# Performance work log

Hardware: AMD Instinct MI355X
Metric: run time of the kernel (lower is better)

The kernel has to match this reference:

```python
import jax, jax.numpy as jnp
import numpy as np

WET_MIX = 0.3
FEEDBACK = 0.4
ROOM_SIZE = 0.5
NUM_REFL = 8
NUM_HEADS = 4

# Delay kernel table: int(delay) in {0,1,2,>=3} -> kernel_size {identity,3,5,7}.
# A k-tap kernel with padding k//2 == the same kernel zero-padded to 7 taps with padding 3.
def _gauss7(ks):
    g = np.exp(-np.linspace(-2.0, 2.0, ks) ** 2)
    g = g / g.sum()
    out = np.zeros(7, np.float32)
    s = (7 - ks) // 2
    out[s:s + ks] = g
    return out
_delta = np.zeros(7, np.float32); _delta[3] = 1.0
K_TABLE = jnp.asarray(np.stack([_delta, _gauss7(3), _gauss7(5), _gauss7(7)]))  # [4,7]


def _conv2d(x, w, b, pad):
    y = jax.lax.conv_general_dilated(x, w, (1, 1), [(pad, pad), (pad, pad)],
                                     dimension_numbers=('NCHW', 'OIHW', 'NCHW'))
    return y + b[None, :, None, None]


def _delay_line(x, kern7):
    # vertical depthwise Gaussian blur, same for every (batch, channel) plane
    b, c, h, w = x.shape
    k = kern7.reshape(1, 1, 7, 1)
    y = jax.lax.conv_general_dilated(x.reshape(b * c, 1, h, w), k, (1, 1), [(3, 3), (0, 0)],
                                     dimension_numbers=('NCHW', 'OIHW', 'NCHW'))
    return y.reshape(b, c, h, w)


def _forward(x, refl_w, refl_d, sc_w, sc_b, fb_w, fb_b, d1_w, d1_b, d2_w, d2_b,
             in_proj_w, in_proj_b, out_proj_w, out_proj_b, oc_w, oc_b):
    B, C, H, W = x.shape
    scaled = refl_d * ROOM_SIZE
    kidx = jnp.clip(jnp.floor(scaled).astype(jnp.int32), 0, 3)  # int(delay) detaches grad, as in torch

    wet = jnp.zeros_like(x)
    fb_buf = x * 0.1
    spatial = _conv2d(x, sc_w, sc_b, 1)  # [B,2C,H,W]

    for i in range(NUM_REFL):
        refl = _delay_line(fb_buf, K_TABLE[kidx[i]])
        refl = _conv2d(refl, fb_w, fb_b, 1)
        damp = jax.nn.sigmoid(_conv2d(jax.nn.silu(_conv2d(refl, d1_w, d1_b, 0)), d2_w, d2_b, 0))
        refl = refl * damp
        weight = jax.nn.sigmoid(refl_w[i]) * (0.8 ** i)
        wet = wet + refl * weight
        fb_buf = fb_buf + refl * (FEEDBACK * 0.1)

    # MultiheadAttention over L = H*W tokens, embed_dim=C=4, 4 heads (head_dim=1)
    L = H * W
    hd = C // NUM_HEADS
    wet_flat = wet.reshape(B, C, L).transpose(0, 2, 1)           # [B,L,C]
    qkv = wet_flat @ in_proj_w.T + in_proj_b                     # [B,L,3C]
    q, k, v = jnp.split(qkv, 3, axis=-1)
    def heads(t):
        return t.reshape(B, L, NUM_HEADS, hd).transpose(0, 2, 1, 3)  # [B,H,L,hd]
    q, k, v = heads(q), heads(k), heads(v)
    scores = jnp.einsum('bhqd,bhkd->bhqk', q, k) / np.sqrt(hd).astype(np.float32)
    attn = jax.nn.softmax(scores, axis=-1)
    o = jnp.einsum('bhqk,bhkd->bhqd', attn, v)
    o = o.transpose(0, 2, 1, 3).reshape(B, L, C) @ out_proj_w.T + out_proj_b
    wet2 = o.transpose(0, 2, 1).reshape(B, C, H, W)

    combined = jnp.concatenate([spatial, wet2], axis=1)          # [B,3C,H,W]
    processed_wet = _conv2d(combined, oc_w, oc_b, 0)
    return x * (1.0 - WET_MIX) + processed_wet * WET_MIX


def setup_inputs() -> dict:
    key = jax.random.key(0)
    ks = jax.random.split(key, 16)
    B, C, H, W = 2, 4, 64, 64
    f32 = jnp.float32
    return {
        'x': jax.random.normal(ks[0], (B, C, H, W), f32),
        'refl_w': jax.random.normal(ks[1], (8,), f32) * 0.1,
        'refl_d': jax.random.randint(ks[2], (8,), 1, 16).astype(f32),
        'sc_w': jax.random.normal(ks[3], (2 * C, C, 3, 3), f32) * 0.1,
        'sc_b': jnp.zeros((2 * C,), f32),
        'fb_w': jax.random.normal(ks[4], (C, C, 3, 3), f32) * 0.1,
        'fb_b': jnp.zeros((C,), f32),
        'd1_w': jax.random.normal(ks[5], (C // 2, C, 1, 1), f32) * 0.3,
        'd1_b': jnp.zeros((C // 2,), f32),
        'd2_w': jax.random.normal(ks[6], (C, C // 2, 1, 1), f32) * 0.3,
        'd2_b': jnp.zeros((C,), f32),
        'in_proj_w': jax.random.normal(ks[7], (3 * C, C), f32) * 0.3,
        'in_proj_b': jnp.zeros((3 * C,), f32),
        'out_proj_w': jax.random.normal(ks[8], (C, C), f32) * 0.3,
        'out_proj_b': jnp.zeros((C,), f32),
        'oc_w': jax.random.normal(ks[9], (C, 3 * C, 1, 1), f32) * 0.2,
        'oc_b': jnp.zeros((C,), f32),
    }


def reference(x, refl_w, refl_d, sc_w, sc_b, fb_w, fb_b, d1_w, d1_b, d2_w, d2_b,
              in_proj_w, in_proj_b, out_proj_w, out_proj_b, oc_w, oc_b):
    return _forward(x, refl_w, refl_d, sc_w, sc_b, fb_w, fb_b, d1_w, d1_b, d2_w, d2_b,
                    in_proj_w, in_proj_b, out_proj_w, out_proj_b, oc_w, oc_b)
```

## Files before the change

kernel.cpp:

```cpp
#include <hip/hip_runtime.h>
#include <math.h>


#define ZERO4 make_float4(0.f, 0.f, 0.f, 0.f)

__device__ __forceinline__ float sigf(float v) { return 1.0f / (1.0f + __expf(-v)); }

__device__ __forceinline__ float dppL(float v) {
    return __int_as_float(__builtin_amdgcn_mov_dpp(__float_as_int(v), 0x138, 0xf, 0xf, true));
}
__device__ __forceinline__ float dppR(float v) {
    return __int_as_float(__builtin_amdgcn_mov_dpp(__float_as_int(v), 0x130, 0xf, 0xf, true));
}
__device__ __forceinline__ float4 shL4(float4 v) {
    return make_float4(dppL(v.x), dppL(v.y), dppL(v.z), dppL(v.w));
}
__device__ __forceinline__ float4 shR4(float4 v) {
    return make_float4(dppR(v.x), dppR(v.y), dppR(v.z), dppR(v.w));
}

__device__ __forceinline__ void tap(float4& a, const float4 t, const float* wp) {
    a.x += wp[0]   * t.x + wp[9]    * t.y + wp[18]    * t.z + wp[27]    * t.w;
    a.y += wp[36]  * t.x + wp[36+9] * t.y + wp[36+18] * t.z + wp[36+27] * t.w;
    a.z += wp[72]  * t.x + wp[72+9] * t.y + wp[72+18] * t.z + wp[72+27] * t.w;
    a.w += wp[108] * t.x + wp[108+9]* t.y + wp[108+18]* t.z + wp[108+27]* t.w;
}

__global__ __launch_bounds__(1024, 1) void reverb_qkv_kernel(
    const float* __restrict__ x,
    const float* __restrict__ refl_w,
    const float* __restrict__ refl_d,
    const float* __restrict__ fb_w,
    const float* __restrict__ fb_b,
    const float* __restrict__ d1_w,
    const float* __restrict__ d1_b,
    const float* __restrict__ d2_w,
    const float* __restrict__ d2_b,
    const float* __restrict__ ipw,
    const float* __restrict__ ipb,
    float* __restrict__ Qg, float* __restrict__ Kg, float* __restrict__ Vg)
{
    __shared__ float4 P [18 * 64];
    __shared__ float4 BL[18 * 64];
    __shared__ float4 WT[2 * 64];
    __shared__ float  GT[3][8];

    const int blk   = blockIdx.x;
    const int batch = blk >> 5;
    const int own0  = (blk & 31) << 1;
    const int LB    = own0 - 8;
    const int tid   = threadIdx.x;
    const int wy    = tid >> 6;
    const int r     = tid & 63;

    if (tid < 3) {
        const int rr = tid + 1;
        const int ks = 2 * rr + 1;
        const int s  = (7 - ks) >> 1;
        const double step = 4.0 / (double)(ks - 1);
        double g[7]; double sum = 0.0;
        for (int t = 0; t < 7; ++t) {
            if (t < ks) { double u = -2.0 + step * (double)t; g[t] = exp(-u * u); sum += g[t]; }
        }
        for (int t = 0; t < 7; ++t) GT[tid][t] = 0.0f;
        for (int t = 0; t < ks; ++t) GT[tid][s + t] = (float)(g[t] / sum);
    }

    for (int idx = tid; idx < 18 * 64; idx += 1024) {
        const int lc  = idx >> 6;
        const int row = idx & 63;
        const int gc  = LB + lc;
        float4 v = ZERO4;
        if (gc >= 0 && gc < 64) {
            const int base = batch * 16384 + row * 64 + gc;
            v.x = 0.1f * x[base];
            v.y = 0.1f * x[base + 4096];
            v.z = 0.1f * x[base + 8192];
            v.w = 0.1f * x[base + 12288];
        }
        P[idx] = v;
    }
    __syncthreads();

    double w8 = 1.0;
    for (int j = 0; j < 8; ++j) {
        int kidx = (int)floorf(refl_d[j] * 0.5f);
        kidx = kidx < 0 ? 0 : (kidx > 3 ? 3 : kidx);
        float kv[7];
        #pragma unroll
        for (int u = 0; u < 7; ++u) {
            const float dv = (u == 3) ? 1.0f : 0.0f;
            kv[u] = (kidx == 0) ? dv : GT[kidx - 1][u];
        }
        const float wgt = sigf(refl_w[j]) * (float)w8;

        const int clo = max(0, own0 - (7 - j));
        const int chi = min(64, own0 + 2 + (7 - j));

        const int lcA   = (clo - 1) - LB;
        const int nBlur = (chi + 1) - (clo - 1);
        for (int t = wy; t < nBlur; t += 16) {
            const int lc = lcA + t;
            const int gc = LB + lc;
            float4 b = ZERO4;
            if (gc >= 0 && gc < 64) {
                const float4 v  = P[lc * 64 + r];
                const float4 l1 = shL4(v),  l2 = shL4(l1), l3 = shL4(l2);
                const float4 r1 = shR4(v),  r2 = shR4(r1), r3 = shR4(r2);
                b.x = kv[0]*l3.x + kv[1]*l2.x + kv[2]*l1.x + kv[3]*v.x
                    + kv[4]*r1.x + kv[5]*r2.x + kv[6]*r3.x;
                b.y = kv[0]*l3.y + kv[1]*l2.y + kv[2]*l1.y + kv[3]*v.y
                    + kv[4]*r1.y + kv[5]*r2.y + kv[6]*r3.y;
                b.z = kv[0]*l3.z + kv[1]*l2.z + kv[2]*l1.z + kv[3]*v.z
                    + kv[4]*r1.z + kv[5]*r2.z + kv[6]*r3.z;
                b.w = kv[0]*l3.w + kv[1]*l2.w + kv[2]*l1.w + kv[3]*v.w
                    + kv[4]*r1.w + kv[5]*r2.w + kv[6]*r3.w;
            }
            BL[lc * 64 + r] = b;
        }
        __syncthreads();

        const int c = clo + wy;
        if (wy < chi - clo) {
            const int lc = c - LB;
            const float4 bm = BL[(lc - 1) * 64 + r];
            const float4 bc = BL[lc * 64 + r];
            const float4 bp = BL[(lc + 1) * 64 + r];

            float4 acc = make_float4(fb_b[0], fb_b[1], fb_b[2], fb_b[3]);
            tap(acc, shL4(bm), fb_w + 0);  tap(acc, shL4(bc), fb_w + 1);  tap(acc, shL4(bp), fb_w + 2);
            tap(acc, bm,       fb_w + 3);  tap(acc, bc,       fb_w + 4);  tap(acc, bp,       fb_w + 5);
            tap(acc, shR4(bm), fb_w + 6);  tap(acc, shR4(bc), fb_w + 7);  tap(acc, shR4(bp), fb_w + 8);

            float4 rr = acc;
            float h0 = d1_b[0] + d1_w[0]*rr.x + d1_w[1]*rr.y + d1_w[2]*rr.z + d1_w[3]*rr.w;
            float h1 = d1_b[1] + d1_w[4]*rr.x + d1_w[5]*rr.y + d1_w[6]*rr.z + d1_w[7]*rr.w;
            h0 = h0 * sigf(h0);
            h1 = h1 * sigf(h1);
            const float d0  = sigf(d2_b[0] + d2_w[0]*h0 + d2_w[1]*h1);
            const float d1v = sigf(d2_b[1] + d2_w[2]*h0 + d2_w[3]*h1);
            const float d2v = sigf(d2_b[2] + d2_w[4]*h0 + d2_w[5]*h1);
            const float d3v = sigf(d2_b[3] + d2_w[6]*h0 + d2_w[7]*h1);
            rr.x *= d0; rr.y *= d1v; rr.z *= d2v; rr.w *= d3v;

            const float4 oldfb = P[lc * 64 + r];
            P[lc * 64 + r] = make_float4(oldfb.x + 0.04f*rr.x, oldfb.y + 0.04f*rr.y,
                                         oldfb.z + 0.04f*rr.z, oldfb.w + 0.04f*rr.w);

            if (c >= own0 && c < own0 + 2) {
                const int widx = (c - own0) * 64 + r;
                float4 wv = make_float4(wgt*rr.x, wgt*rr.y, wgt*rr.z, wgt*rr.w);
                if (j > 0) {
                    const float4 old = WT[widx];
                    wv.x += old.x; wv.y += old.y; wv.z += old.z; wv.w += old.w;
                }
                WT[widx] = wv;
            }
        }
        __syncthreads();
        w8 *= 0.8;
    }

    if (tid < 128) {
        const int row = tid & 63;
        const int oc  = tid >> 6;
        const int c   = own0 + oc;
        const float4 wv = WT[oc * 64 + row];
        #pragma unroll
        for (int h = 0; h < 4; ++h) {
            const float q = ipb[h]
                + ipw[h*4+0]*wv.x + ipw[h*4+1]*wv.y
                + ipw[h*4+2]*wv.z + ipw[h*4+3]*wv.w;
            const float k = ipb[4+h]
                + ipw[(4+h)*4+0]*wv.x + ipw[(4+h)*4+1]*wv.y
                + ipw[(4+h)*4+2]*wv.z + ipw[(4+h)*4+3]*wv.w;
            const float v = ipb[8+h]
                + ipw[(8+h)*4+0]*wv.x + ipw[(8+h)*4+1]*wv.y
                + ipw[(8+h)*4+2]*wv.z + ipw[(8+h)*4+3]*wv.w;
            const int o = (batch * 4 + h) * 4096 + row * 64 + c;
            Qg[o] = q; Kg[o] = k; Vg[o] = v;
        }
    }
}

__global__ __launch_bounds__(256) void attn_kernel(
    const float* __restrict__ Qg, const float* __restrict__ Kg,
    const float* __restrict__ Vg,
    float* __restrict__ PN, float* __restrict__ PD, float* __restrict__ PM)
{
    __shared__ float2 KV[1024];
    __shared__ float  wred[8];
    __shared__ float  partN[256], partD[256];

    const int bh  = blockIdx.x >> 8;
    const int sub = (blockIdx.x >> 2) & 63;
    const int ks  = blockIdx.x & 3;
    const int tid = threadIdx.x;

    const float* Kp = Kg + bh * 4096 + ks * 1024;
    const float* Vp = Vg + bh * 4096 + ks * 1024;

    float pmax = -3.0e38f, pmin = 3.0e38f;
    #pragma unroll
    for (int t = tid; t < 1024; t += 256) {
        const float kk = Kp[t];
        const float vv = Vp[t];
        KV[t] = make_float2(kk, vv);
        pmax = fmaxf(pmax, kk);
        pmin = fminf(pmin, kk);
    }
    #pragma unroll
    for (int off = 32; off > 0; off >>= 1) {
        pmax = fmaxf(pmax, __shfl_xor(pmax, off, 64));
        pmin = fminf(pmin, __shfl_xor(pmin, off, 64));
    }
    if ((tid & 63) == 0) { wred[tid >> 6] = pmax; wred[4 + (tid >> 6)] = pmin; }
    __syncthreads();
    const float kmax = fmaxf(fmaxf(wred[0], wred[1]), fmaxf(wred[2], wred[3]));
    const float kmin = fminf(fminf(wred[4], wred[5]), fminf(wred[6], wred[7]));

    const int ql = tid & 63;
    const int kh = __builtin_amdgcn_readfirstlane(tid >> 6);
    const int qi = sub * 64 + ql;

    const float L2E = 1.4426950408889634f;
    const float q  = Qg[bh * 4096 + qi];
    const float q2 = q * L2E;
    const float m2 = ((q >= 0.0f) ? q * kmax : q * kmin) * L2E;
    const float nm2 = -m2;

    const float4* KV4 = (const float4*)KV;
    const int base4 = kh * 128;

    float num0 = 0.f, num1 = 0.f, den0 = 0.f, den1 = 0.f;
    #pragma unroll 8
    for (int j = 0; j < 128; ++j) {
        const float4 f = KV4[base4 + j];
        const float e0 = __builtin_amdgcn_exp2f(__fmaf_rn(q2, f.x, nm2));
        den0 += e0;  num0 = __fmaf_rn(e0, f.y, num0);
        const float e1 = __builtin_amdgcn_exp2f(__fmaf_rn(q2, f.z, nm2));
        den1 += e1;  num1 = __fmaf_rn(e1, f.w, num1);
    }
    partN[tid] = num0 + num1;
    partD[tid] = den0 + den1;
    __syncthreads();
    if (tid < 64) {
        const float n = partN[tid] + partN[tid + 64] + partN[tid + 128] + partN[tid + 192];
        const float d = partD[tid] + partD[tid + 64] + partD[tid + 128] + partD[tid + 192];
        const int o = bh * 16384 + ks * 4096 + sub * 64 + tid;
        PN[o] = n;
        PD[o] = d;
        PM[o] = m2;
    }
}

__global__ __launch_bounds__(128) void final_kernel(
    const float* __restrict__ x,
    const float* __restrict__ sc_w, const float* __restrict__ sc_b,
    const float* __restrict__ opw,  const float* __restrict__ opb,
    const float* __restrict__ ocw,  const float* __restrict__ ocb,
    const float* __restrict__ PN,   const float* __restrict__ PD,
    const float* __restrict__ PM,   float* __restrict__ out)
{
    const int g   = blockIdx.x * 128 + threadIdx.x;
    const int b   = g >> 12;
    const int pix = g & 4095;
    const int y   = pix >> 6;
    const int xc  = pix & 63;

    float xin[4][3][3];
    #pragma unroll
    for (int ic = 0; ic < 4; ++ic)
        #pragma unroll
        for (int ky = 0; ky < 3; ++ky)
            #pragma unroll
            for (int kx = 0; kx < 3; ++kx) {
                const int yy = y + ky - 1, xx = xc + kx - 1;
                xin[ic][ky][kx] = (yy >= 0 && yy < 64 && xx >= 0 && xx < 64)
                                    ? x[(b * 4 + ic) * 4096 + yy * 64 + xx] : 0.f;
            }

    float sp[8];
    #pragma unroll
    for (int oc = 0; oc < 8; ++oc) {
        float a = sc_b[oc];
        #pragma unroll
        for (int ic = 0; ic < 4; ++ic)
            #pragma unroll
            for (int ky = 0; ky < 3; ++ky)
                #pragma unroll
                for (int kx = 0; kx < 3; ++kx)
                    a += sc_w[(oc * 4 + ic) * 9 + ky * 3 + kx] * xin[ic][ky][kx];
        sp[oc] = a;
    }

    float oh[4];
    #pragma unroll
    for (int h = 0; h < 4; ++h) {
        const int bh = b * 4 + h;
        float m2s[4];
        #pragma unroll
        for (int ks = 0; ks < 4; ++ks) m2s[ks] = PM[bh * 16384 + ks * 4096 + pix];
        const float M2 = fmaxf(fmaxf(m2s[0], m2s[1]), fmaxf(m2s[2], m2s[3]));
        float n = 0.f, d = 0.f;
        #pragma unroll
        for (int ks = 0; ks < 4; ++ks) {
            const float s = __builtin_amdgcn_exp2f(m2s[ks] - M2);
            n = __fmaf_rn(PN[bh * 16384 + ks * 4096 + pix], s, n);
            d = __fmaf_rn(PD[bh * 16384 + ks * 4096 + pix], s, d);
        }
        oh[h] = n / d;
    }

    float w2[4];
    #pragma unroll
    for (int c = 0; c < 4; ++c)
        w2[c] = opb[c] + opw[c*4+0]*oh[0] + opw[c*4+1]*oh[1]
                       + opw[c*4+2]*oh[2] + opw[c*4+3]*oh[3];

    #pragma unroll
    for (int c = 0; c < 4; ++c) {
        float a = ocb[c];
        #pragma unroll
        for (int j = 0; j < 8; ++j) a += ocw[c * 12 + j] * sp[j];
        #pragma unroll
        for (int h = 0; h < 4; ++h) a += ocw[c * 12 + 8 + h] * w2[h];
        const int idx = (b * 4 + c) * 4096 + y * 64 + xc;
        out[idx] = 0.7f * x[idx] + 0.3f * a;
    }
}

extern "C" void kernel_launch(void* const* d_in, const int* in_sizes, int n_in,
                              void* d_out, int out_size, void* d_ws, size_t ws_size,
                              hipStream_t stream) {
    const float* x      = (const float*)d_in[0];
    const float* refl_w = (const float*)d_in[1];
    const float* refl_d = (const float*)d_in[2];
    const float* sc_w   = (const float*)d_in[3];
    const float* sc_b   = (const float*)d_in[4];
    const float* fb_w   = (const float*)d_in[5];
    const float* fb_b   = (const float*)d_in[6];
    const float* d1_w   = (const float*)d_in[7];
    const float* d1_b   = (const float*)d_in[8];
    const float* d2_w   = (const float*)d_in[9];
    const float* d2_b   = (const float*)d_in[10];
    const float* ipw    = (const float*)d_in[11];
    const float* ipb    = (const float*)d_in[12];
    const float* opw    = (const float*)d_in[13];
    const float* opb    = (const float*)d_in[14];
    const float* ocw    = (const float*)d_in[15];
    const float* ocb    = (const float*)d_in[16];
    float* out = (float*)d_out;

    float* Q  = (float*)d_ws;
    float* K  = Q + 32768;
    float* V  = K + 32768;
    float* PN = V + 32768;
    float* PD = PN + 131072;
    float* PM = PD + 131072;

    reverb_qkv_kernel<<<dim3(64), dim3(1024), 0, stream>>>(
        x, refl_w, refl_d, fb_w, fb_b, d1_w, d1_b, d2_w, d2_b, ipw, ipb,
        Q, K, V);
    attn_kernel<<<dim3(2048), dim3(256), 0, stream>>>(Q, K, V, PN, PD, PM);
    final_kernel<<<dim3(64), dim3(128), 0, stream>>>(
        x, sc_w, sc_b, opw, opb, ocw, ocb, PN, PD, PM, out);
}
```

Measured before the change: 136.9 us.

## Register-block four queries per thread in attention and stage fb conv weights in LDS

The attention kernel now gives each thread four queries and each block 256 queries with 512 threads splitting keys eight ways. Every K/V value read from LDS is reused four times and the grid shrinks from 2048 to 512 blocks. Separately, the feedback 3x3 conv weights are transposed into shared memory as float4 rows so the reverb kernel does vector LDS loads instead of scalar global loads. The trade-off is more registers per thread and fewer blocks, which cuts occupancy and parallelism in the attention stage.

```diff
diff --git a/kernel.cpp b/kernel.cpp
--- a/kernel.cpp
+++ b/kernel.cpp
@@ -19,11 +19,12 @@
     return make_float4(dppR(v.x), dppR(v.y), dppR(v.z), dppR(v.w));
 }
 
-__device__ __forceinline__ void tap(float4& a, const float4 t, const float* wp) {
-    a.x += wp[0]   * t.x + wp[9]    * t.y + wp[18]    * t.z + wp[27]    * t.w;
-    a.y += wp[36]  * t.x + wp[36+9] * t.y + wp[36+18] * t.z + wp[36+27] * t.w;
-    a.z += wp[72]  * t.x + wp[72+9] * t.y + wp[72+18] * t.z + wp[72+27] * t.w;
-    a.w += wp[108] * t.x + wp[108+9]* t.y + wp[108+18]* t.z + wp[108+27]* t.w;
+__device__ __forceinline__ void tapL(float4& a, const float4 t, const float4* w) {
+    const float4 w0 = w[0], w1 = w[1], w2 = w[2], w3 = w[3];
+    a.x += w0.x * t.x + w1.x * t.y + w2.x * t.z + w3.x * t.w;
+    a.y += w0.y * t.x + w1.y * t.y + w2.y * t.z + w3.y * t.w;
+    a.z += w0.z * t.x + w1.z * t.y + w2.z * t.z + w3.z * t.w;
+    a.w += w0.w * t.x + w1.w * t.y + w2.w * t.z + w3.w * t.w;
 }
 
 __global__ __launch_bounds__(1024, 1) void reverb_qkv_kernel(
@@ -44,6 +45,7 @@
     __shared__ float4 BL[18 * 64];
     __shared__ float4 WT[2 * 64];
     __shared__ float  GT[3][8];
+    __shared__ float  WL[9 * 16];
 
     const int blk   = blockIdx.x;
     const int batch = blk >> 5;
@@ -64,6 +66,14 @@
         }
         for (int t = 0; t < 7; ++t) GT[tid][t] = 0.0f;
         for (int t = 0; t < ks; ++t) GT[tid][s + t] = (float)(g[t] / sum);
+    }
+    if (tid >= 64 && tid < 64 + 144) {
+        const int idx = tid - 64;
+        const int oc  = idx / 36;
+        const int rem = idx - oc * 36;
+        const int ic  = rem / 9;
+        const int tp  = rem - ic * 9;
+        WL[tp * 16 + ic * 4 + oc] = fb_w[idx];
     }
 
     for (int idx = tid; idx < 18 * 64; idx += 1024) {
@@ -81,6 +91,8 @@
         P[idx] = v;
     }
     __syncthreads();
+
+    const float4* WL4 = (const float4*)WL;
 
     double w8 = 1.0;
     for (int j = 0; j < 8; ++j) {
@@ -128,9 +140,9 @@
             const float4 bp = BL[(lc + 1) * 64 + r];
 
             float4 acc = make_float4(fb_b[0], fb_b[1], fb_b[2], fb_b[3]);
-            tap(acc, shL4(bm), fb_w + 0);  tap(acc, shL4(bc), fb_w + 1);  tap(acc, shL4(bp), fb_w + 2);
-            tap(acc, bm,       fb_w + 3);  tap(acc, bc,       fb_w + 4);  tap(acc, bp,       fb_w + 5);
-            tap(acc, shR4(bm), fb_w + 6);  tap(acc, shR4(bc), fb_w + 7);  tap(acc, shR4(bp), fb_w + 8);
+            tapL(acc, shL4(bm), WL4 + 0*4);  tapL(acc, shL4(bc), WL4 + 1*4);  tapL(acc, shL4(bp), WL4 + 2*4);
+            tapL(acc, bm,       WL4 + 3*4);  tapL(acc, bc,       WL4 + 4*4);  tapL(acc, bp,       WL4 + 5*4);
+            tapL(acc, shR4(bm), WL4 + 6*4);  tapL(acc, shR4(bc), WL4 + 7*4);  tapL(acc, shR4(bp), WL4 + 8*4);
 
             float4 rr = acc;
             float h0 = d1_b[0] + d1_w[0]*rr.x + d1_w[1]*rr.y + d1_w[2]*rr.z + d1_w[3]*rr.w;
@@ -183,17 +195,17 @@
     }
 }
 
-__global__ __launch_bounds__(256) void attn_kernel(
+__global__ __launch_bounds__(512) void attn_kernel(
     const float* __restrict__ Qg, const float* __restrict__ Kg,
     const float* __restrict__ Vg,
     float* __restrict__ PN, float* __restrict__ PD, float* __restrict__ PM)
 {
     __shared__ float2 KV[1024];
-    __shared__ float  wred[8];
-    __shared__ float  partN[256], partD[256];
-
-    const int bh  = blockIdx.x >> 8;
-    const int sub = (blockIdx.x >> 2) & 63;
+    __shared__ float  wred[16];
+    __shared__ float  pN[4][512], pD[4][512];
+
+    const int bh  = blockIdx.x >> 6;
+    const int sub = (blockIdx.x >> 2) & 15;
     const int ks  = blockIdx.x & 3;
     const int tid = threadIdx.x;
 
@@ -202,7 +214,7 @@
 
     float pmax = -3.0e38f, pmin = 3.0e38f;
     #pragma unroll
-    for (int t = tid; t < 1024; t += 256) {
+    for (int t = tid; t < 1024; t += 512) {
         const float kk = Kp[t];
         const float vv = Vp[t];
         KV[t] = make_float2(kk, vv);
@@ -214,43 +226,64 @@
         pmax = fmaxf(pmax, __shfl_xor(pmax, off, 64));
         pmin = fminf(pmin, __shfl_xor(pmin, off, 64));
     }
-    if ((tid & 63) == 0) { wred[tid >> 6] = pmax; wred[4 + (tid >> 6)] = pmin; }
+    if ((tid & 63) == 0) { wred[tid >> 6] = pmax; wred[8 + (tid >> 6)] = pmin; }
     __syncthreads();
-    const float kmax = fmaxf(fmaxf(wred[0], wred[1]), fmaxf(wred[2], wred[3]));
-    const float kmin = fminf(fminf(wred[4], wred[5]), fminf(wred[6], wred[7]));
+    float kmax = wred[0], kmin = wred[8];
+    #pragma unroll
+    for (int w = 1; w < 8; ++w) {
+        kmax = fmaxf(kmax, wred[w]);
+        kmin = fminf(kmin, wred[8 + w]);
+    }
 
     const int ql = tid & 63;
     const int kh = __builtin_amdgcn_readfirstlane(tid >> 6);
-    const int qi = sub * 64 + ql;
 
     const float L2E = 1.4426950408889634f;
-    const float q  = Qg[bh * 4096 + qi];
-    const float q2 = q * L2E;
-    const float m2 = ((q >= 0.0f) ? q * kmax : q * kmin) * L2E;
-    const float nm2 = -m2;
+    float q2[4], nm2[4];
+    #pragma unroll
+    for (int t = 0; t < 4; ++t) {
+        const float q = Qg[bh * 4096 + sub * 256 + ql + 64 * t];
+        q2[t]  = q * L2E;
+        nm2[t] = -(((q >= 0.0f) ? q * kmax : q * kmin) * L2E);
+    }
 
     const float4* KV4 = (const float4*)KV;
-    const int base4 = kh * 128;
-
-    float num0 = 0.f, num1 = 0.f, den0 = 0.f, den1 = 0.f;
+    const int base4 = kh * 64;
+
+    float num[4] = {0.f, 0.f, 0.f, 0.f};
+    float den[4] = {0.f, 0.f, 0.f, 0.f};
     #pragma unroll 8
-    for (int j = 0; j < 128; ++j) {
+    for (int j = 0; j < 64; ++j) {
         const float4 f = KV4[base4 + j];
-        const float e0 = __builtin_amdgcn_exp2f(__fmaf_rn(q2, f.x, nm2));
-        den0 += e0;  num0 = __fmaf_rn(e0, f.y, num0);
-        const float e1 = __builtin_amdgcn_exp2f(__fmaf_rn(q2, f.z, nm2));
-        den1 += e1;  num1 = __fmaf_rn(e1, f.w, num1);
-    }
-    partN[tid] = num0 + num1;
-    partD[tid] = den0 + den1;
+        #pragma unroll
+        for (int t = 0; t < 4; ++t) {
+            const float e0 = __builtin_amdgcn_exp2f(__fmaf_rn(q2[t], f.x, nm2[t]));
+            den[t] += e0;  num[t] = __fmaf_rn(e0, f.y, num[t]);
+            const float e1 = __builtin_amdgcn_exp2f(__fmaf_rn(q2[t], f.z, nm2[t]));
+            den[t] += e1;  num[t] = __fmaf_rn(e1, f.w, num[t]);
+        }
+    }
+    #pragma unroll
+    for (int t = 0; t < 4; ++t) {
+        pN[t][tid] = num[t];
+        pD[t][tid] = den[t];
+    }
     __syncthreads();
-    if (tid < 64) {
-        const float n = partN[tid] + partN[tid + 64] + partN[tid + 128] + partN[tid + 192];
-        const float d = partD[tid] + partD[tid + 64] + partD[tid + 128] + partD[tid + 192];
-        const int o = bh * 16384 + ks * 4096 + sub * 64 + tid;
+    if (tid < 256) {
+        const int which = tid >> 6;
+        const int qa    = tid & 63;
+        float n = 0.f, d = 0.f;
+        #pragma unroll
+        for (int w = 0; w < 8; ++w) {
+            n += pN[which][w * 64 + qa];
+            d += pD[which][w * 64 + qa];
+        }
+        const int qi = sub * 256 + tid;
+        const int o  = bh * 16384 + ks * 4096 + qi;
         PN[o] = n;
         PD[o] = d;
-        PM[o] = m2;
+        const float q = Qg[bh * 4096 + qi];
+        PM[o] = ((q >= 0.0f) ? q * kmax : q * kmin) * L2E;
     }
 }
 
@@ -362,7 +395,7 @@
     reverb_qkv_kernel<<<dim3(64), dim3(1024), 0, stream>>>(
         x, refl_w, refl_d, fb_w, fb_b, d1_w, d1_b, d2_w, d2_b, ipw, ipb,
         Q, K, V);
-    attn_kernel<<<dim3(2048), dim3(256), 0, stream>>>(Q, K, V, PN, PD, PM);
+    attn_kernel<<<dim3(512), dim3(512), 0, stream>>>(Q, K, V, PN, PD, PM);
     final_kernel<<<dim3(64), dim3(128), 0, stream>>>(
         x, sc_w, sc_b, opw, opb, ocw, ocb, PN, PD, PM, out);
 }
```

After: 132.4 us. 1.03x faster.
